# Kernel optimization log

Measured on AMD Instinct MI355X. Metric: run time of the kernel, lower is better.

Reference implementation:

```python
import jax, jax.numpy as jnp
import numpy as np


def setup_inputs() -> dict:
    key = jax.random.key(0)
    ks = jax.random.split(key, 6)
    B, C, H, W = 8, 256, 32, 32
    d = C // 8  # 32
    return {
        "x": jax.random.normal(ks[0], (B, C, H, W), dtype=jnp.float32),
        "Wq": jax.random.normal(ks[1], (d, C), dtype=jnp.float32) * 0.05,
        "bq": jnp.zeros((d,), dtype=jnp.float32),
        "Wk": jax.random.normal(ks[2], (d, C), dtype=jnp.float32) * 0.05,
        "bk": jnp.zeros((d,), dtype=jnp.float32),
        "Wv": jax.random.normal(ks[3], (C, C), dtype=jnp.float32) * 0.05,
        "bv": jnp.zeros((C,), dtype=jnp.float32),
        "Wr": jax.random.normal(ks[4], (d, 2), dtype=jnp.float32) * 0.05,
        "br": jnp.zeros((d,), dtype=jnp.float32),
        "gamma": jnp.array([0.5], dtype=jnp.float32),
    }


def reference(x, Wq, bq, Wk, bk, Wv, bv, Wr, br, gamma):
    B, C, H, W = x.shape
    N = H * W
    d = Wq.shape[0]
    xf = x.reshape(B, C, N)

    # 1x1 convs == per-pixel linear projections
    q = jnp.einsum('dc,bcn->bdn', Wq, xf) + bq[None, :, None]  # (B,d,N)
    k = jnp.einsum('dc,bcn->bdn', Wk, xf) + bk[None, :, None]  # (B,d,N)
    v = jnp.einsum('oc,bcn->bon', Wv, xf) + bv[None, :, None]  # (B,C,N)

    # relative position code: pairwise coord diffs through 1x1 conv (batch-independent)
    gh, gw = jnp.meshgrid(jnp.linspace(0.0, 1.0, H), jnp.linspace(0.0, 1.0, W), indexing='ij')
    coords = jnp.stack([gh.reshape(-1), gw.reshape(-1)])  # (2,N)
    diff = coords[:, :, None] - coords[:, None, :]         # (2,N,N)
    rp_code = jnp.einsum('dt,tij->dij', Wr, diff) + br[:, None, None]  # (d,N,N)

    scale = 1.0 / jnp.sqrt(jnp.asarray(d, dtype=x.dtype))
    score = jnp.einsum('bdi,bdj->bij', q, k) * scale          # (B,N,N)
    rp_score = jnp.einsum('bdi,dij->bij', q, rp_code) * scale  # (B,N,N)
    attn = jax.nn.softmax(score + rp_score, axis=-1)

    # out[b,c,i] = sum_j v[b,c,j] * attn[b,i,j]
    out = jnp.einsum('bcj,bij->bci', v, attn)
    return gamma[0] * out.reshape(B, C, H, W) + x
```

## Files before the change

### kernel.cpp

```cpp
#include <hip/hip_runtime.h>
#include <hip/hip_bf16.h>

#define BATCH 8
#define CH    256
#define NN    1024
#define DD    32

#define QT_OFF 0
#define KT_OFF (BATCH * NN * DD)
#define V_OFF  (2 * BATCH * NN * DD)
#define V2_B   (NN * CH)

#define SCALE 0.17677669529663687f
#define INV31 (1.0f / 31.0f)

typedef __attribute__((ext_vector_type(4))) float f32x4;
typedef __attribute__((ext_vector_type(8))) short bf16x8;

__device__ __forceinline__ unsigned int packbf2(float lo, float hi) {
    __hip_bfloat162 h = __float22bfloat162_rn(make_float2(lo, hi));
    union { __hip_bfloat162 h; unsigned int u; } cv; cv.h = h;
    return cv.u;
}
__device__ __forceinline__ unsigned short f2bf(float x) {
    union { float f; unsigned int u; } v; v.f = x;
    return (unsigned short)((v.u + 0x7FFFu + ((v.u >> 16) & 1u)) >> 16);
}

__global__ __launch_bounds__(256) void proj_kernel(
    const float* __restrict__ x,
    const float* __restrict__ Wq, const float* __restrict__ bq,
    const float* __restrict__ Wk, const float* __restrict__ bk,
    const float* __restrict__ Wv, const float* __restrict__ bv,
    const float* __restrict__ Wr,
    unsigned short* __restrict__ ws)
{
    const int nt   = blockIdx.x;
    const int b    = blockIdx.y;
    const int tid  = threadIdx.x;
    const int wv   = tid >> 6;
    const int lane = tid & 63;
    const int n16  = lane & 15;
    const int q4   = lane >> 4;
    const int n    = nt * 16 + n16;

    f32x4 acc[5];
#pragma unroll
    for (int t = 0; t < 5; t++) acc[t] = (f32x4){0.f, 0.f, 0.f, 0.f};

    const float* wrow[5];
#pragma unroll
    for (int t = 0; t < 5; t++) {
        const int m = (wv * 5 + t) * 16 + n16;
        wrow[t] = (m < 32) ? (Wq + m * CH)
                : (m < 64) ? (Wk + (m - 32) * CH)
                           : (Wv + (m - 64) * CH);
    }

    for (int c0 = 0; c0 < CH; c0 += 32) {
        const int kofs = c0 + q4 * 8;
        float bx[8];
#pragma unroll
        for (int jj = 0; jj < 8; jj++)
            bx[jj] = x[(size_t)(b * CH + kofs + jj) * NN + n];
        union { unsigned int u[4]; bf16x8 v; } bf;
#pragma unroll
        for (int p = 0; p < 4; p++) bf.u[p] = packbf2(bx[2 * p], bx[2 * p + 1]);

#pragma unroll
        for (int t = 0; t < 5; t++) {
            const float* wp = wrow[t] + kofs;
            const float4 a0 = *(const float4*)(wp);
            const float4 a1 = *(const float4*)(wp + 4);
            union { unsigned int u[4]; bf16x8 v; } af;
            af.u[0] = packbf2(a0.x, a0.y); af.u[1] = packbf2(a0.z, a0.w);
            af.u[2] = packbf2(a1.x, a1.y); af.u[3] = packbf2(a1.z, a1.w);
            acc[t] = __builtin_amdgcn_mfma_f32_16x16x32_bf16(af.v, bf.v, acc[t], 0, 0, 0);
        }
    }

    const int jt  = n >> 5;
    const int q4p = (n >> 3) & 3;
    const int jj  = n & 7;
#pragma unroll
    for (int t = 0; t < 5; t++) {
        const int mf = wv * 5 + t;
        const int mb = mf * 16 + q4 * 4;
        if (mb < 32) {
            const float r0 = (acc[t][0] + bq[mb + 0]) * SCALE;
            const float r1 = (acc[t][1] + bq[mb + 1]) * SCALE;
            const float r2 = (acc[t][2] + bq[mb + 2]) * SCALE;
            const float r3 = (acc[t][3] + bq[mb + 3]) * SCALE;
            uint2 st = { packbf2(r0, r1), packbf2(r2, r3) };
            *(uint2*)(ws + QT_OFF + (size_t)(b * NN + n) * DD + mb) = st;
        } else if (mb < 64) {
            const int d = mb - 32;
            const float An = (float)(n >> 5) * INV31;
            const float Bn = (float)(n & 31) * INV31;
            float r[4];
#pragma unroll
            for (int rr = 0; rr < 4; rr++)
                r[rr] = acc[t][rr] + bk[d + rr] - An * Wr[2 * (d + rr)] - Bn * Wr[2 * (d + rr) + 1];
            uint2 st = { packbf2(r[0], r[1]), packbf2(r[2], r[3]) };
            *(uint2*)(ws + KT_OFF + (size_t)(b * NN + n) * DD + d) = st;
        } else {
            const int c = mb - 64;
#pragma unroll
            for (int rr = 0; rr < 4; rr++) {
                const int cc = c + rr;
                const size_t off = V_OFF + (size_t)b * V2_B
                                 + (size_t)jt * 8192 + (size_t)(cc >> 4) * 512
                                 + (size_t)(q4p * 16 + (cc & 15)) * 8 + jj;
                ws[off] = f2bf(acc[t][rr] + bv[cc]);
            }
        }
    }
}

__global__ __launch_bounds__(512) void attn_kernel(
    const float* __restrict__ x,
    const float* __restrict__ gamma,
    const unsigned short* __restrict__ ws,
    float* __restrict__ out)
{
    const int it   = blockIdx.x;
    const int b    = blockIdx.y;
    const int tid  = threadIdx.x;
    const int wv   = (tid >> 6) & 3;
    const int jh   = tid >> 8;
    const int lane = tid & 63;
    const int n    = lane & 15;
    const int q4   = lane >> 4;
    const int i0   = it * 16;
    const int cb   = wv * 64;

    __shared__ float accL[4 * 16 * 64];
    __shared__ float lL[16];

    const unsigned short* qT = ws + QT_OFF + (size_t)b * NN * DD;
    const unsigned short* kT = ws + KT_OFF + (size_t)b * NN * DD + (size_t)jh * 512 * DD;
    const unsigned short* vb = ws + V_OFF + (size_t)b * V2_B
                             + (size_t)jh * 16 * 8192 + (size_t)wv * 4 * 512
                             + (size_t)lane * 8;

    const bf16x8 qf = *(const bf16x8*)(qT + (size_t)(i0 + n) * DD + q4 * 8);

    f32x4 acc[4];
#pragma unroll
    for (int t = 0; t < 4; t++) acc[t] = (f32x4){0.f, 0.f, 0.f, 0.f};
    float lsum = 0.f;

    bf16x8 ka0 = *(const bf16x8*)(kT + (size_t)(n) * DD + q4 * 8);
    bf16x8 ka1 = *(const bf16x8*)(kT + (size_t)(16 + n) * DD + q4 * 8);
    bf16x8 va[4];
#pragma unroll
    for (int t = 0; t < 4; t++)
        va[t] = *(const bf16x8*)(vb + t * 512);

    const int qh2 = (q4 & 1) * 2;

#pragma unroll 4
    for (int ch = 0; ch < 16; ch++) {
        const bf16x8 ka0c = ka0, ka1c = ka1;
        bf16x8 vac[4];
#pragma unroll
        for (int t = 0; t < 4; t++) vac[t] = va[t];

        {
            const int j0 = (ch + 1) * 32;
            ka0 = *(const bf16x8*)(kT + (size_t)(j0 + n) * DD + q4 * 8);
            ka1 = *(const bf16x8*)(kT + (size_t)(j0 + 16 + n) * DD + q4 * 8);
#pragma unroll
            for (int t = 0; t < 4; t++)
                va[t] = *(const bf16x8*)(vb + (ch + 1) * 8192 + t * 512);
        }

        const f32x4 z = {0.f, 0.f, 0.f, 0.f};
        f32x4 s0 = __builtin_amdgcn_mfma_f32_16x16x32_bf16(ka0c, qf, z, 0, 0, 0);
        f32x4 s1 = __builtin_amdgcn_mfma_f32_16x16x32_bf16(ka1c, qf, z, 0, 0, 0);

        float p0[4], p1[4];
#pragma unroll
        for (int r = 0; r < 4; r++) {
            p0[r] = __expf(s0[r]);
            p1[r] = __expf(s1[r]);
            lsum += p0[r] + p1[r];
        }

        unsigned int pk0[2] = { packbf2(p0[0], p0[1]), packbf2(p0[2], p0[3]) };
        unsigned int pk1[2] = { packbf2(p1[0], p1[1]), packbf2(p1[2], p1[3]) };
        union { unsigned int u[4]; bf16x8 v; } pf;
#pragma unroll
        for (int t = 0; t < 4; t++) {
            const int src = (qh2 + (t >> 1)) * 16 + n;
            const unsigned int lo = (unsigned int)__shfl((int)pk0[t & 1], src, 64);
            const unsigned int hi = (unsigned int)__shfl((int)pk1[t & 1], src, 64);
            pf.u[t] = (q4 >= 2) ? hi : lo;
        }

#pragma unroll
        for (int t = 0; t < 4; t++)
            acc[t] = __builtin_amdgcn_mfma_f32_16x16x32_bf16(vac[t], pf.v, acc[t], 0, 0, 0);
    }

    lsum += __shfl_xor(lsum, 16, 64);
    lsum += __shfl_xor(lsum, 32, 64);

    if (jh == 1) {
#pragma unroll
        for (int t = 0; t < 4; t++)
#pragma unroll
            for (int r = 0; r < 4; r++)
                accL[(wv * 16 + t * 4 + r) * 64 + lane] = acc[t][r];
        if (wv == 0 && lane < 16) lL[lane] = lsum;
    }
    __syncthreads();

    if (jh == 0) {
        const float ltot = lsum + lL[n];
        const float rl = gamma[0] / ltot;
#pragma unroll
        for (int t = 0; t < 4; t++) {
#pragma unroll
            for (int r = 0; r < 4; r++) {
                const float a = acc[t][r] + accL[(wv * 16 + t * 4 + r) * 64 + lane];
                const int c = cb + t * 16 + q4 * 4 + r;
                const size_t idx = (size_t)(b * CH + c) * NN + i0 + n;
                out[idx] = a * rl + x[idx];
            }
        }
    }
}

extern "C" void kernel_launch(void* const* d_in, const int* in_sizes, int n_in,
                              void* d_out, int out_size, void* d_ws, size_t ws_size,
                              hipStream_t stream) {
    (void)in_sizes; (void)n_in; (void)out_size; (void)ws_size;
    const float* x     = (const float*)d_in[0];
    const float* Wq    = (const float*)d_in[1];
    const float* bq    = (const float*)d_in[2];
    const float* Wk    = (const float*)d_in[3];
    const float* bk    = (const float*)d_in[4];
    const float* Wv    = (const float*)d_in[5];
    const float* bv    = (const float*)d_in[6];
    const float* Wr    = (const float*)d_in[7];
    const float* gamma = (const float*)d_in[9];
    float* out = (float*)d_out;
    unsigned short* ws = (unsigned short*)d_ws;

    proj_kernel<<<dim3(64, 8), 256, 0, stream>>>(x, Wq, bq, Wk, bk, Wv, bv, Wr, ws);
    attn_kernel<<<dim3(64, 8), 512, 0, stream>>>(x, gamma, ws, out);
}
```

Before: 119.5 us.

## Process 32 query rows per attention block and fold log2e into the Q scale

Each attention block now handles two 16-row query tiles and reuses the same K and V fragments for both, halving the grid to 32x8 blocks. This halves the repeated K/V traffic from L2/HBM, which the previous layout re-read once per 16 queries. The Q projection now also multiplies by log2(e), so the softmax can use exp2f instead of __expf. The costs are more registers for the doubled accumulators, a larger shared buffer, and fewer blocks to spread across the CUs.

```diff
diff --git a/kernel.cpp b/kernel.cpp
--- a/kernel.cpp
+++ b/kernel.cpp
@@ -11,7 +11,7 @@
 #define V_OFF  (2 * BATCH * NN * DD)
 #define V2_B   (NN * CH)
 
-#define SCALE 0.17677669529663687f
+#define SCALE_Q (0.17677669529663687f * 1.4426950408889634f)
 #define INV31 (1.0f / 31.0f)
 
 typedef __attribute__((ext_vector_type(4))) float f32x4;
@@ -87,10 +87,10 @@
         const int mf = wv * 5 + t;
         const int mb = mf * 16 + q4 * 4;
         if (mb < 32) {
-            const float r0 = (acc[t][0] + bq[mb + 0]) * SCALE;
-            const float r1 = (acc[t][1] + bq[mb + 1]) * SCALE;
-            const float r2 = (acc[t][2] + bq[mb + 2]) * SCALE;
-            const float r3 = (acc[t][3] + bq[mb + 3]) * SCALE;
+            const float r0 = (acc[t][0] + bq[mb + 0]) * SCALE_Q;
+            const float r1 = (acc[t][1] + bq[mb + 1]) * SCALE_Q;
+            const float r2 = (acc[t][2] + bq[mb + 2]) * SCALE_Q;
+            const float r3 = (acc[t][3] + bq[mb + 3]) * SCALE_Q;
             uint2 st = { packbf2(r0, r1), packbf2(r2, r3) };
             *(uint2*)(ws + QT_OFF + (size_t)(b * NN + n) * DD + mb) = st;
         } else if (mb < 64) {
@@ -131,11 +131,11 @@
     const int lane = tid & 63;
     const int n    = lane & 15;
     const int q4   = lane >> 4;
-    const int i0   = it * 16;
+    const int i0   = it * 32;
     const int cb   = wv * 64;
 
-    __shared__ float accL[4 * 16 * 64];
-    __shared__ float lL[16];
+    __shared__ float accL[4 * 32 * 64];
+    __shared__ float lL[32];
 
     const unsigned short* qT = ws + QT_OFF + (size_t)b * NN * DD;
     const unsigned short* kT = ws + KT_OFF + (size_t)b * NN * DD + (size_t)jh * 512 * DD;
@@ -143,12 +143,16 @@
                              + (size_t)jh * 16 * 8192 + (size_t)wv * 4 * 512
                              + (size_t)lane * 8;
 
-    const bf16x8 qf = *(const bf16x8*)(qT + (size_t)(i0 + n) * DD + q4 * 8);
-
-    f32x4 acc[4];
-#pragma unroll
-    for (int t = 0; t < 4; t++) acc[t] = (f32x4){0.f, 0.f, 0.f, 0.f};
-    float lsum = 0.f;
+    const bf16x8 qf0 = *(const bf16x8*)(qT + (size_t)(i0 + n) * DD + q4 * 8);
+    const bf16x8 qf1 = *(const bf16x8*)(qT + (size_t)(i0 + 16 + n) * DD + q4 * 8);
+
+    f32x4 acc0[4], acc1[4];
+#pragma unroll
+    for (int t = 0; t < 4; t++) {
+        acc0[t] = (f32x4){0.f, 0.f, 0.f, 0.f};
+        acc1[t] = (f32x4){0.f, 0.f, 0.f, 0.f};
+    }
+    float lsum0 = 0.f, lsum1 = 0.f;
 
     bf16x8 ka0 = *(const bf16x8*)(kT + (size_t)(n) * DD + q4 * 8);
     bf16x8 ka1 = *(const bf16x8*)(kT + (size_t)(16 + n) * DD + q4 * 8);
@@ -158,6 +162,9 @@
         va[t] = *(const bf16x8*)(vb + t * 512);
 
     const int qh2 = (q4 & 1) * 2;
+    int src[4];
+#pragma unroll
+    for (int t = 0; t < 4; t++) src[t] = (qh2 + (t >> 1)) * 16 + n;
 
 #pragma unroll 4
     for (int ch = 0; ch < 16; ch++) {
@@ -176,57 +183,76 @@
         }
 
         const f32x4 z = {0.f, 0.f, 0.f, 0.f};
-        f32x4 s0 = __builtin_amdgcn_mfma_f32_16x16x32_bf16(ka0c, qf, z, 0, 0, 0);
-        f32x4 s1 = __builtin_amdgcn_mfma_f32_16x16x32_bf16(ka1c, qf, z, 0, 0, 0);
-
-        float p0[4], p1[4];
+        f32x4 s0a = __builtin_amdgcn_mfma_f32_16x16x32_bf16(ka0c, qf0, z, 0, 0, 0);
+        f32x4 s1a = __builtin_amdgcn_mfma_f32_16x16x32_bf16(ka1c, qf0, z, 0, 0, 0);
+        f32x4 s0b = __builtin_amdgcn_mfma_f32_16x16x32_bf16(ka0c, qf1, z, 0, 0, 0);
+        f32x4 s1b = __builtin_amdgcn_mfma_f32_16x16x32_bf16(ka1c, qf1, z, 0, 0, 0);
+
+        float p0a[4], p1a[4], p0b[4], p1b[4];
 #pragma unroll
         for (int r = 0; r < 4; r++) {
-            p0[r] = __expf(s0[r]);
-            p1[r] = __expf(s1[r]);
-            lsum += p0[r] + p1[r];
-        }
-
-        unsigned int pk0[2] = { packbf2(p0[0], p0[1]), packbf2(p0[2], p0[3]) };
-        unsigned int pk1[2] = { packbf2(p1[0], p1[1]), packbf2(p1[2], p1[3]) };
-        union { unsigned int u[4]; bf16x8 v; } pf;
+            p0a[r] = exp2f(s0a[r]);
+            p1a[r] = exp2f(s1a[r]);
+            p0b[r] = exp2f(s0b[r]);
+            p1b[r] = exp2f(s1b[r]);
+            lsum0 += p0a[r] + p1a[r];
+            lsum1 += p0b[r] + p1b[r];
+        }
+
+        unsigned int pk0a[2] = { packbf2(p0a[0], p0a[1]), packbf2(p0a[2], p0a[3]) };
+        unsigned int pk1a[2] = { packbf2(p1a[0], p1a[1]), packbf2(p1a[2], p1a[3]) };
+        unsigned int pk0b[2] = { packbf2(p0b[0], p0b[1]), packbf2(p0b[2], p0b[3]) };
+        unsigned int pk1b[2] = { packbf2(p1b[0], p1b[1]), packbf2(p1b[2], p1b[3]) };
+        union { unsigned int u[4]; bf16x8 v; } pfa, pfb;
 #pragma unroll
         for (int t = 0; t < 4; t++) {
-            const int src = (qh2 + (t >> 1)) * 16 + n;
-            const unsigned int lo = (unsigned int)__shfl((int)pk0[t & 1], src, 64);
-            const unsigned int hi = (unsigned int)__shfl((int)pk1[t & 1], src, 64);
-            pf.u[t] = (q4 >= 2) ? hi : lo;
-        }
-
+            const unsigned int loa = (unsigned int)__shfl((int)pk0a[t & 1], src[t], 64);
+            const unsigned int hia = (unsigned int)__shfl((int)pk1a[t & 1], src[t], 64);
+            const unsigned int lob = (unsigned int)__shfl((int)pk0b[t & 1], src[t], 64);
+            const unsigned int hib = (unsigned int)__shfl((int)pk1b[t & 1], src[t], 64);
+            pfa.u[t] = (q4 >= 2) ? hia : loa;
+            pfb.u[t] = (q4 >= 2) ? hib : lob;
+        }
+
+#pragma unroll
+        for (int t = 0; t < 4; t++) {
+            acc0[t] = __builtin_amdgcn_mfma_f32_16x16x32_bf16(vac[t], pfa.v, acc0[t], 0, 0, 0);
+            acc1[t] = __builtin_amdgcn_mfma_f32_16x16x32_bf16(vac[t], pfb.v, acc1[t], 0, 0, 0);
+        }
+    }
+
+    lsum0 += __shfl_xor(lsum0, 16, 64);
+    lsum0 += __shfl_xor(lsum0, 32, 64);
+    lsum1 += __shfl_xor(lsum1, 16, 64);
+    lsum1 += __shfl_xor(lsum1, 32, 64);
+
+    if (jh == 1) {
 #pragma unroll
         for (int t = 0; t < 4; t++)
-            acc[t] = __builtin_amdgcn_mfma_f32_16x16x32_bf16(vac[t], pf.v, acc[t], 0, 0, 0);
-    }
-
-    lsum += __shfl_xor(lsum, 16, 64);
-    lsum += __shfl_xor(lsum, 32, 64);
-
-    if (jh == 1) {
-#pragma unroll
-        for (int t = 0; t < 4; t++)
-#pragma unroll
-            for (int r = 0; r < 4; r++)
-                accL[(wv * 16 + t * 4 + r) * 64 + lane] = acc[t][r];
-        if (wv == 0 && lane < 16) lL[lane] = lsum;
+#pragma unroll
+            for (int r = 0; r < 4; r++) {
+                accL[(wv * 32 + t * 4 + r) * 64 + lane]      = acc0[t][r];
+                accL[(wv * 32 + 16 + t * 4 + r) * 64 + lane] = acc1[t][r];
+            }
+        if (wv == 0 && lane < 16) lL[lane] = lsum0;
+        if (wv == 1 && lane < 16) lL[16 + lane] = lsum1;
     }
     __syncthreads();
 
     if (jh == 0) {
-        const float ltot = lsum + lL[n];
-        const float rl = gamma[0] / ltot;
+        const float g = gamma[0];
+        const float rl0 = g / (lsum0 + lL[n]);
+        const float rl1 = g / (lsum1 + lL[16 + n]);
 #pragma unroll
         for (int t = 0; t < 4; t++) {
 #pragma unroll
             for (int r = 0; r < 4; r++) {
-                const float a = acc[t][r] + accL[(wv * 16 + t * 4 + r) * 64 + lane];
                 const int c = cb + t * 16 + q4 * 4 + r;
-                const size_t idx = (size_t)(b * CH + c) * NN + i0 + n;
-                out[idx] = a * rl + x[idx];
+                const size_t base = (size_t)(b * CH + c) * NN + i0 + n;
+                const float a0 = acc0[t][r] + accL[(wv * 32 + t * 4 + r) * 64 + lane];
+                const float a1 = acc1[t][r] + accL[(wv * 32 + 16 + t * 4 + r) * 64 + lane];
+                out[base]      = a0 * rl0 + x[base];
+                out[base + 16] = a1 * rl1 + x[base + 16];
             }
         }
     }
@@ -249,5 +275,5 @@
     unsigned short* ws = (unsigned short*)d_ws;
 
     proj_kernel<<<dim3(64, 8), 256, 0, stream>>>(x, Wq, bq, Wk, bk, Wv, bv, Wr, ws);
-    attn_kernel<<<dim3(64, 8), 512, 0, stream>>>(x, gamma, ws, out);
-}
+    attn_kernel<<<dim3(32, 8), 512, 0, stream>>>(x, gamma, ws, out);
+}
```

After: 117.7 us. About the same (-1.5%).
